# Kernel tuning notes

Hardware: AMD Instinct MI355X
Metric: run time of the kernel (lower is better)

Reference implementation:

```python
import jax, jax.numpy as jnp
import numpy as np

B, T, C = 2, 2048, 1024
H = 16
HD = C // H  # head_size = 64
FF = 4 * C
EPS = 1e-5


def layernorm(x, g, b):
    mu = jnp.mean(x, axis=-1, keepdims=True)
    var = jnp.mean(jnp.square(x - mu), axis=-1, keepdims=True)
    return (x - mu) * jax.lax.rsqrt(var + EPS) * g + b


def setup_inputs() -> dict:
    key = jax.random.key(0)
    ks = jax.random.split(key, 12)
    s_c = 1.0 / np.sqrt(C)
    s_hc = 1.0 / np.sqrt(C)
    s_ff = 1.0 / np.sqrt(FF)
    return {
        "x": jax.random.normal(ks[0], (B, T, C), jnp.float32),
        "Wq": jax.random.normal(ks[1], (H, C, HD), jnp.float32) * s_hc,
        "Wk": jax.random.normal(ks[2], (H, C, HD), jnp.float32) * s_hc,
        "Wv": jax.random.normal(ks[3], (H, C, HD), jnp.float32) * s_hc,
        "Wo": jax.random.normal(ks[4], (C, C), jnp.float32) * s_c,
        "bo": jax.random.normal(ks[5], (C,), jnp.float32) * 0.01,
        "W1": jax.random.normal(ks[6], (C, FF), jnp.float32) * s_c,
        "b1": jax.random.normal(ks[7], (FF,), jnp.float32) * 0.01,
        "W2": jax.random.normal(ks[8], (FF, C), jnp.float32) * s_ff,
        "b2": jax.random.normal(ks[9], (C,), jnp.float32) * 0.01,
        "g1": jnp.ones((C,), jnp.float32),
        "be1": jnp.zeros((C,), jnp.float32),
        "g2": jnp.ones((C,), jnp.float32),
        "be2": jnp.zeros((C,), jnp.float32),
    }


def reference(x, Wq, Wk, Wv, Wo, bo, W1, b1, W2, b2, g1, be1, g2, be2):
    # --- self-attention sublayer (pre-LN, residual) ---
    h = layernorm(x, g1, be1)                               # [B,T,C]
    q = jnp.einsum("btc,hcd->bhtd", h, Wq)                   # [B,H,T,HD]
    k = jnp.einsum("btc,hcd->bhtd", h, Wk)
    v = jnp.einsum("btc,hcd->bhtd", h, Wv)
    scores = jnp.einsum("bhtd,bhsd->bhts", q, k) * (HD ** -0.5)
    causal = jnp.tril(jnp.ones((T, T), bool))
    scores = jnp.where(causal, scores, -jnp.inf)
    wei = jax.nn.softmax(scores, axis=-1)                    # [B,H,T,T]
    attn = jnp.einsum("bhts,bhsd->bhtd", wei, v)             # [B,H,T,HD]
    attn = attn.transpose(0, 2, 1, 3).reshape(B, T, H * HD)  # concat heads
    x = x + attn @ Wo + bo
    # --- feedforward sublayer (pre-LN, residual) ---
    h2 = layernorm(x, g2, be2)
    x = x + jax.nn.relu(h2 @ W1 + b1) @ W2 + b2
    return x
```

## Files before the change

kernel.cpp:

```cpp
#include <hip/hip_runtime.h>
#include <hip/hip_bf16.h>
#include <cstdint>
#include <cstddef>
#include <cstring>

#define B_ 2
#define T_ 2048
#define C_ 1024
#define H_ 16
#define HD_ 64
#define FF_ 4096
#define BT_ (B_*T_)

typedef __attribute__((ext_vector_type(8))) short short8;
typedef __attribute__((ext_vector_type(4))) float f32x4;

__device__ __forceinline__ float bf2f(ushort u) {
    return __uint_as_float(((uint)u) << 16);
}
__device__ __forceinline__ ushort f2bf(float f) {
    uint x = __float_as_uint(f);
    return (ushort)((x + 0x7fffu + ((x >> 16) & 1u)) >> 16);
}
__device__ __forceinline__ ushort f2bf_hw(float f) {
    __hip_bfloat16 h = __float2bfloat16(f);
    ushort u;
    __builtin_memcpy(&u, &h, 2);
    return u;
}

#define GLDS16(g, l)                                                        \
    __builtin_amdgcn_global_load_lds(                                       \
        (const __attribute__((address_space(1))) void*)(g),                 \
        (__attribute__((address_space(3))) void*)(l), 16, 0, 0)

__global__ __launch_bounds__(256) void ln_kernel(const float* __restrict__ x,
                                                 const float* __restrict__ g,
                                                 const float* __restrict__ b,
                                                 ushort* __restrict__ out) {
    int row = blockIdx.x;
    int tid = threadIdx.x;
    const float* xr = x + (size_t)row * C_;
    float4 v = *(const float4*)(xr + tid * 4);
    float s = v.x + v.y + v.z + v.w;
    float q = v.x*v.x + v.y*v.y + v.z*v.z + v.w*v.w;
    #pragma unroll
    for (int off = 32; off > 0; off >>= 1) {
        s += __shfl_down(s, off);
        q += __shfl_down(q, off);
    }
    __shared__ float ss[4], qs[4];
    if ((tid & 63) == 0) { ss[tid >> 6] = s; qs[tid >> 6] = q; }
    __syncthreads();
    s = ss[0] + ss[1] + ss[2] + ss[3];
    q = qs[0] + qs[1] + qs[2] + qs[3];
    float mu  = s * (1.0f / C_);
    float var = q * (1.0f / C_) - mu * mu;
    float r = rsqrtf(var + 1e-5f);
    float4 gv = *(const float4*)(g + tid * 4);
    float4 bv = *(const float4*)(b + tid * 4);
    ushort4 o;
    o.x = f2bf((v.x - mu) * r * gv.x + bv.x);
    o.y = f2bf((v.y - mu) * r * gv.y + bv.y);
    o.z = f2bf((v.z - mu) * r * gv.z + bv.z);
    o.w = f2bf((v.w - mu) * r * gv.w + bv.w);
    *(ushort4*)(out + (size_t)row * C_ + tid * 4) = o;
}

__global__ __launch_bounds__(256) void tcvt_w(const float* __restrict__ Wo,
                                              const float* __restrict__ W1,
                                              const float* __restrict__ W2,
                                              ushort* __restrict__ Wo_t,
                                              ushort* __restrict__ W1_t,
                                              ushort* __restrict__ W2_t) {
    __shared__ float tile[32][33];
    int fb = blockIdx.x;
    const float* in;
    ushort* out;
    int Cc, ldo, bx, by;
    if (fb < 1024) {
        in = Wo; out = Wo_t; Cc = 1024; ldo = 1024;
        bx = fb & 31; by = fb >> 5;
    } else if (fb < 5120) {
        int t = fb - 1024;
        in = W1; out = W1_t; Cc = 4096; ldo = 1024;
        bx = t & 127; by = t >> 7;
    } else {
        int t = fb - 5120;
        in = W2; out = W2_t; Cc = 1024; ldo = 4096;
        bx = t & 31; by = t >> 5;
    }
    int c0 = bx * 32, r0 = by * 32;
    int tx = threadIdx.x & 31, ty = threadIdx.x >> 5;
    #pragma unroll
    for (int i = 0; i < 4; i++) {
        int r = ty + i * 8;
        tile[r][tx] = in[(size_t)(r0 + r) * Cc + c0 + tx];
    }
    __syncthreads();
    #pragma unroll
    for (int i = 0; i < 4; i++) {
        int c = ty + i * 8;
        out[(size_t)(c0 + c) * ldo + r0 + tx] = f2bf(tile[tx][c]);
    }
}

__global__ __launch_bounds__(256) void tcvt_qkv(const float* __restrict__ Wq,
                                                const float* __restrict__ Wk,
                                                const float* __restrict__ Wv,
                                                ushort* __restrict__ qkvw) {
    __shared__ float tile[32][33];
    int z = blockIdx.z;
    const float* in = (z < 16 ? Wq : (z < 32 ? Wk : Wv)) + (size_t)(z & 15) * 65536;
    ushort* out = qkvw + (size_t)z * 65536;
    int c0 = blockIdx.x * 32, r0 = blockIdx.y * 32;
    #pragma unroll
    for (int i = 0; i < 4; i++) {
        int r = threadIdx.y + i * 8;
        tile[r][threadIdx.x] = in[(size_t)(r0 + r) * 64 + c0 + threadIdx.x];
    }
    __syncthreads();
    #pragma unroll
    for (int i = 0; i < 4; i++) {
        int c = threadIdx.y + i * 8;
        out[(size_t)(c0 + c) * 1024 + r0 + threadIdx.x] = f2bf(tile[threadIdx.x][c]);
    }
}

template<int EPI, bool OUT_BF16>
__global__ __launch_bounds__(512, 4) void gemm2(
    const ushort* __restrict__ A,
    const ushort* __restrict__ Bt,
    void* __restrict__ Cout,
    const float* __restrict__ bias,
    const float* __restrict__ resid,
    int M, int N, int K, int KS)
{
    __shared__ ushort As[3][128 * 32];
    __shared__ ushort Bs[3][256 * 32];

    int gx = gridDim.x;
    int nwg = gx * gridDim.y;
    int bid = blockIdx.y * gx + blockIdx.x;
    int cpx = nwg >> 3;
    int swz = (bid & 7) * cpx + (bid >> 3);
    int bx = swz % gx, by = swz / gx;

    int tid  = threadIdx.x;
    int lane = tid & 63;
    int lr = lane & 15, lq = lane >> 4;
    int wave = tid >> 6;
    int wr = wave >> 2, wc = wave & 3;
    int m0 = by * 128, n0 = bx * 256;
    int Koff = blockIdx.z * KS;
    size_t zoff = (size_t)blockIdx.z * ((size_t)M * N);

    f32x4 acc[4][4];
    #pragma unroll
    for (int i = 0; i < 4; i++)
        #pragma unroll
        for (int j = 0; j < 4; j++)
            acc[i][j] = {0.f, 0.f, 0.f, 0.f};

    int srow = tid >> 2;
    int scol = ((tid & 3) ^ ((srow >> 1) & 3)) * 8;
    const ushort* gA  = A  + (size_t)(m0 + srow) * K + Koff + scol;
    const ushort* gB0 = Bt + (size_t)(n0 + srow) * K + Koff + scol;
    const ushort* gB1 = Bt + (size_t)(n0 + 128 + srow) * K + Koff + scol;
    int NT = KS / 32;

    auto stage = [&](int kt, int buf) {
        int off = kt * 32;
        GLDS16(gA + off,  (char*)As[buf] + wave * 1024);
        GLDS16(gB0 + off, (char*)Bs[buf] + wave * 1024);
        GLDS16(gB1 + off, (char*)Bs[buf] + 8192 + wave * 1024);
    };

    stage(0, 0);
    stage(1, 1);
    asm volatile("s_waitcnt vmcnt(3)" ::: "memory");
    __builtin_amdgcn_s_barrier();

    int so = (lq ^ ((lr >> 1) & 3)) << 4;

    int cur = 0;
    for (int t = 0; t < NT; ++t) {
        const char* Ab = (const char*)As[cur] + (wr * 64 + lr) * 64 + so;
        const char* Bb = (const char*)Bs[cur] + (wc * 64 + lr) * 64 + so;

        short8 a[4], b[4];
        #pragma unroll
        for (int fr = 0; fr < 4; fr++)
            a[fr] = *(const short8*)(Ab + fr * 1024);
        #pragma unroll
        for (int fc = 0; fc < 4; fc++)
            b[fc] = *(const short8*)(Bb + fc * 1024);

        if (t + 2 < NT) {
            int nb = cur + 2;
            if (nb >= 3) nb -= 3;
            stage(t + 2, nb);
        }

        #pragma unroll
        for (int fr = 0; fr < 4; fr++)
            #pragma unroll
            for (int fc = 0; fc < 4; fc++)
                acc[fr][fc] = __builtin_amdgcn_mfma_f32_16x16x32_bf16(
                    a[fr], b[fc], acc[fr][fc], 0, 0, 0);

        if (t + 1 == NT) break;
        if (t + 2 < NT)
            asm volatile("s_waitcnt vmcnt(3)" ::: "memory");
        else
            asm volatile("s_waitcnt vmcnt(0)" ::: "memory");
        __builtin_amdgcn_s_barrier();
        cur = (cur == 2) ? 0 : cur + 1;
    }

    #pragma unroll
    for (int fr = 0; fr < 4; fr++) {
        #pragma unroll
        for (int fc = 0; fc < 4; fc++) {
            int col = n0 + wc * 64 + fc * 16 + lr;
            #pragma unroll
            for (int j = 0; j < 4; j++) {
                int row = m0 + wr * 64 + fr * 16 + lq * 4 + j;
                float v = acc[fr][fc][j];
                if (EPI & 1) v += bias[col];
                if (EPI & 2) v = fmaxf(v, 0.f);
                if (EPI & 4) v += resid[(size_t)row * N + col];
                if (OUT_BF16)
                    ((ushort*)Cout)[zoff + (size_t)row * N + col] = f2bf(v);
                else
                    ((float*)Cout)[zoff + (size_t)row * N + col] = v;
            }
        }
    }
}

__global__ __launch_bounds__(512, 4) void gemm_qkvt(
    const ushort* __restrict__ h_bf,
    const ushort* __restrict__ qkvw,
    ushort* __restrict__ qk_act,
    ushort* __restrict__ p_vt)
{
    __shared__ ushort As[3][128 * 32];
    __shared__ ushort Bs[3][256 * 32];

    const ushort* A; const ushort* Bt; ushort* Cb;
    int N, K, KS, gx, nwg, bid, Koff;
    size_t zoff;
    int fb = blockIdx.x;
    if (fb < 256) {
        A = h_bf; Bt = qkvw; Cb = qk_act;
        N = 2048; K = C_; KS = C_;
        gx = 8; nwg = 256; bid = fb; Koff = 0; zoff = 0;
    } else {
        int local = fb - 256;
        int z = local >> 7;
        A = qkvw + (size_t)2 * 1024 * 1024; Bt = h_bf; Cb = p_vt;
        N = BT_; K = C_; KS = 512;
        gx = 16; nwg = 128; bid = local & 127;
        Koff = z * 512; zoff = (size_t)z * ((size_t)1024 * BT_);
    }
    int cpx = nwg >> 3;
    int swz = (bid & 7) * cpx + (bid >> 3);
    int bx = swz % gx, by = swz / gx;

    int tid  = threadIdx.x;
    int lane = tid & 63;
    int lr = lane & 15, lq = lane >> 4;
    int wave = tid >> 6;
    int wr = wave >> 2, wc = wave & 3;
    int m0 = by * 128, n0 = bx * 256;

    f32x4 acc[4][4];
    #pragma unroll
    for (int i = 0; i < 4; i++)
        #pragma unroll
        for (int j = 0; j < 4; j++)
            acc[i][j] = {0.f, 0.f, 0.f, 0.f};

    int srow = tid >> 2;
    int scol = ((tid & 3) ^ ((srow >> 1) & 3)) * 8;
    const ushort* gA  = A  + (size_t)(m0 + srow) * K + Koff + scol;
    const ushort* gB0 = Bt + (size_t)(n0 + srow) * K + Koff + scol;
    const ushort* gB1 = Bt + (size_t)(n0 + 128 + srow) * K + Koff + scol;
    int NT = KS / 32;

    auto stage = [&](int kt, int buf) {
        int off = kt * 32;
        GLDS16(gA + off,  (char*)As[buf] + wave * 1024);
        GLDS16(gB0 + off, (char*)Bs[buf] + wave * 1024);
        GLDS16(gB1 + off, (char*)Bs[buf] + 8192 + wave * 1024);
    };

    stage(0, 0);
    stage(1, 1);
    asm volatile("s_waitcnt vmcnt(3)" ::: "memory");
    __builtin_amdgcn_s_barrier();

    int so = (lq ^ ((lr >> 1) & 3)) << 4;

    int cur = 0;
    for (int t = 0; t < NT; ++t) {
        const char* Ab = (const char*)As[cur] + (wr * 64 + lr) * 64 + so;
        const char* Bb = (const char*)Bs[cur] + (wc * 64 + lr) * 64 + so;

        short8 a[4], b[4];
        #pragma unroll
        for (int fr = 0; fr < 4; fr++)
            a[fr] = *(const short8*)(Ab + fr * 1024);
        #pragma unroll
        for (int fc = 0; fc < 4; fc++)
            b[fc] = *(const short8*)(Bb + fc * 1024);

        if (t + 2 < NT) {
            int nb = cur + 2;
            if (nb >= 3) nb -= 3;
            stage(t + 2, nb);
        }

        #pragma unroll
        for (int fr = 0; fr < 4; fr++)
            #pragma unroll
            for (int fc = 0; fc < 4; fc++)
                acc[fr][fc] = __builtin_amdgcn_mfma_f32_16x16x32_bf16(
                    a[fr], b[fc], acc[fr][fc], 0, 0, 0);

        if (t + 1 == NT) break;
        if (t + 2 < NT)
            asm volatile("s_waitcnt vmcnt(3)" ::: "memory");
        else
            asm volatile("s_waitcnt vmcnt(0)" ::: "memory");
        __builtin_amdgcn_s_barrier();
        cur = (cur == 2) ? 0 : cur + 1;
    }

    #pragma unroll
    for (int fr = 0; fr < 4; fr++) {
        #pragma unroll
        for (int fc = 0; fc < 4; fc++) {
            int col = n0 + wc * 64 + fc * 16 + lr;
            #pragma unroll
            for (int j = 0; j < 4; j++) {
                int row = m0 + wr * 64 + fr * 16 + lq * 4 + j;
                Cb[zoff + (size_t)row * N + col] = f2bf(acc[fr][fc][j]);
            }
        }
    }
}

__global__ __launch_bounds__(256) void vt_red(ushort* __restrict__ vt,
                                              const ushort* __restrict__ p) {
    size_t i = (size_t)blockIdx.x * 256 + threadIdx.x;
    ushort4 a = ((const ushort4*)p)[i];
    ushort4 b = ((const ushort4*)(p + (size_t)1024 * BT_))[i];
    ushort4 o;
    o.x = f2bf(bf2f(a.x) + bf2f(b.x));
    o.y = f2bf(bf2f(a.y) + bf2f(b.y));
    o.z = f2bf(bf2f(a.z) + bf2f(b.z));
    o.w = f2bf(bf2f(a.w) + bf2f(b.w));
    ((ushort4*)vt)[i] = o;
}

__global__ __launch_bounds__(256) void wo_ln(float* __restrict__ out,
                                             ushort* __restrict__ h,
                                             const ushort* __restrict__ p,
                                             const float* __restrict__ bo,
                                             const float* __restrict__ x,
                                             const float* __restrict__ g,
                                             const float* __restrict__ be) {
    int row = blockIdx.x;
    int tid = threadIdx.x;
    size_t base = (size_t)row * C_ + tid * 4;
    float4 v = *(const float4*)(x + base);
    float4 c = *(const float4*)(bo + tid * 4);
    #pragma unroll
    for (int z = 0; z < 4; z++) {
        ushort4 a = *(const ushort4*)(p + (size_t)z * BT_ * C_ + base);
        v.x += bf2f(a.x); v.y += bf2f(a.y);
        v.z += bf2f(a.z); v.w += bf2f(a.w);
    }
    v.x += c.x; v.y += c.y; v.z += c.z; v.w += c.w;
    *(float4*)(out + base) = v;

    float s = v.x + v.y + v.z + v.w;
    float q = v.x*v.x + v.y*v.y + v.z*v.z + v.w*v.w;
    #pragma unroll
    for (int off = 32; off > 0; off >>= 1) {
        s += __shfl_down(s, off);
        q += __shfl_down(q, off);
    }
    __shared__ float ss[4], qs[4];
    if ((tid & 63) == 0) { ss[tid >> 6] = s; qs[tid >> 6] = q; }
    __syncthreads();
    s = ss[0] + ss[1] + ss[2] + ss[3];
    q = qs[0] + qs[1] + qs[2] + qs[3];
    float mu  = s * (1.0f / C_);
    float var = q * (1.0f / C_) - mu * mu;
    float r = rsqrtf(var + 1e-5f);
    float4 gv = *(const float4*)(g + tid * 4);
    float4 bv = *(const float4*)(be + tid * 4);
    ushort4 o;
    o.x = f2bf((v.x - mu) * r * gv.x + bv.x);
    o.y = f2bf((v.y - mu) * r * gv.y + bv.y);
    o.z = f2bf((v.z - mu) * r * gv.z + bv.z);
    o.w = f2bf((v.w - mu) * r * gv.w + bv.w);
    *(ushort4*)(h + base) = o;
}

__global__ __launch_bounds__(256) void ff2_red4(float* __restrict__ out,
                                                const ushort* __restrict__ p,
                                                const float* __restrict__ b2) {
    size_t i = (size_t)blockIdx.x * 256 + threadIdx.x;
    float4 o = ((float4*)out)[i];
    float4 c = ((const float4*)b2)[i & 255];
    #pragma unroll
    for (int z = 0; z < 4; z++) {
        ushort4 a = ((const ushort4*)(p + (size_t)z * BT_ * C_))[i];
        o.x += bf2f(a.x); o.y += bf2f(a.y);
        o.z += bf2f(a.z); o.w += bf2f(a.w);
    }
    o.x += c.x; o.y += c.y; o.z += c.z; o.w += c.w;
    ((float4*)out)[i] = o;
}

__global__ __launch_bounds__(256, 3) void attn_mfma(const ushort* __restrict__ qk,
                                                    const ushort* __restrict__ vt,
                                                    ushort* __restrict__ Opart,
                                                    float* __restrict__ ml) {
    const float C2 = 0.18033688011f;
    const float THR2 = 12.0f;

    int flat = blockIdx.x;
    int xcd = flat & 7;
    int idx = flat >> 3;
    int bh  = xcd * 4 + (idx & 3);
    int qz  = idx >> 2;
    int qa  = 15 - (qz >> 1);
    int z   = qz & 1;

    int bb = bh >> 4;
    int head = bh & 15;
    int q0 = qa * 128;

    int tid  = threadIdx.x;
    int lane = tid & 63;
    int lr = lane & 15, lq = lane >> 4;
    int wave = tid >> 6;
    int qw = q0 + wave * 32;

    __shared__ ushort Ks[2][64 * 64];
    __shared__ ushort Vs[2][64 * 64];
    __shared__ ushort Ps[4][32 * 64];
    char* pw = (char*)Ps[wave];

    short8 qf[2][2];
    {
        const ushort* qb = qk + ((size_t)(bb * T_ + qw)) * 2048 + head * 64;
        #pragma unroll
        for (int mt = 0; mt < 2; mt++)
            #pragma unroll
            for (int kk = 0; kk < 2; kk++)
                qf[mt][kk] = *(const short8*)(qb + (size_t)(mt*16 + lr) * 2048 + kk*32 + lq*8);
    }

    f32x4 acc[2][4];
    f32x4 lsum[2];
    float m2[2][4];
    #pragma unroll
    for (int mt = 0; mt < 2; mt++) {
        #pragma unroll
        for (int dt = 0; dt < 4; dt++) acc[mt][dt] = {0.f, 0.f, 0.f, 0.f};
        lsum[mt] = {0.f, 0.f, 0.f, 0.f};
        #pragma unroll
        for (int j = 0; j < 4; j++) m2[mt][j] = -INFINITY;
    }

    const short8 onesf = {(short)0x3F80, (short)0x3F80, (short)0x3F80, (short)0x3F80,
                          (short)0x3F80, (short)0x3F80, (short)0x3F80, (short)0x3F80};

    int srow = tid >> 3;
    int ssc = ((tid & 7) ^ (srow & 7)) * 8;
    const ushort* kg0 = qk + ((size_t)(bb * T_ + srow)) * 2048 + 1024 + head * 64 + ssc;
    const ushort* vg0 = vt + ((size_t)(head * 64 + srow)) * 4096 + (size_t)bb * 2048 + ssc;

    auto stage = [&](int it, int buf) {
        int s0 = it * 64;
        char* Kb = (char*)Ks[buf] + wave * 1024;
        char* Vb = (char*)Vs[buf] + wave * 1024;
        GLDS16(kg0 + (size_t)s0 * 2048,        Kb);
        GLDS16(kg0 + (size_t)(s0 + 32) * 2048, Kb + 4096);
        GLDS16(vg0 + s0,                        Vb);
        GLDS16(vg0 + (size_t)32 * 4096 + s0,    Vb + 4096);
    };

    int nt = 2 * (qa + 1);
    stage(z, 0);
    __syncthreads();
    int cur = 0;

    for (int it = z; it < nt; it += 2) {
        if (it + 2 < nt) stage(it + 2, cur ^ 1);

        int s0h = it * 64;
        if (s0h <= qw + 31) {
            const ushort* Kc = Ks[cur];
            const ushort* Vc = Vs[cur];

            f32x4 sa[2][4];
            __builtin_amdgcn_s_setprio(1);
            #pragma unroll
            for (int n = 0; n < 4; n++) {
                int row = n*16 + lr;
                const char* kbase = (const char*)Kc + row*128;
                short8 kf0 = *(const short8*)(kbase + ((lq       ^ (row & 7)) << 4));
                short8 kf1 = *(const short8*)(kbase + (((4 + lq) ^ (row & 7)) << 4));
                #pragma unroll
                for (int mt = 0; mt < 2; mt++) {
                    f32x4 tq = {0.f, 0.f, 0.f, 0.f};
                    tq = __builtin_amdgcn_mfma_f32_16x16x32_bf16(qf[mt][0], kf0, tq, 0, 0, 0);
                    tq = __builtin_amdgcn_mfma_f32_16x16x32_bf16(qf[mt][1], kf1, tq, 0, 0, 0);
                    sa[mt][n] = tq;
                }
            }
            __builtin_amdgcn_s_setprio(0);

            if (s0h + 63 > qw) {
                #pragma unroll
                for (int mt = 0; mt < 2; mt++)
                    #pragma unroll
                    for (int n = 0; n < 4; n++)
                        #pragma unroll
                        for (int j = 0; j < 4; j++) {
                            int scolm = s0h + n*16 + lr;
                            int qrow = qw + mt*16 + lq*4 + j;
                            if (scolm > qrow) sa[mt][n][j] = -INFINITY;
                        }
            }

            float vmax2[2][4];
            bool growf = false;
            #pragma unroll
            for (int mt = 0; mt < 2; mt++) {
                #pragma unroll
                for (int j = 0; j < 4; j++) {
                    float v = fmaxf(fmaxf(sa[mt][0][j], sa[mt][1][j]),
                                    fmaxf(sa[mt][2][j], sa[mt][3][j]));
                    #pragma unroll
                    for (int off = 1; off < 16; off <<= 1)
                        v = fmaxf(v, __shfl_xor(v, off));
                    float v2 = v * C2;
                    vmax2[mt][j] = v2;
                    growf |= (v2 > m2[mt][j] + THR2);
                }
            }
            if (__any(growf)) {
                #pragma unroll
                for (int mt = 0; mt < 2; mt++)
                    #pragma unroll
                    for (int j = 0; j < 4; j++) {
                        float m2n = fmaxf(m2[mt][j], vmax2[mt][j]);
                        float corr = __builtin_amdgcn_exp2f(m2[mt][j] - m2n);
                        m2[mt][j] = m2n;
                        lsum[mt][j] *= corr;
                        #pragma unroll
                        for (int dt = 0; dt < 4; dt++)
                            acc[mt][dt][j] *= corr;
                    }
            }

            #pragma unroll
            for (int mt = 0; mt < 2; mt++)
                #pragma unroll
                for (int n = 0; n < 4; n++)
                    #pragma unroll
                    for (int j = 0; j < 4; j++) {
                        float p = __builtin_amdgcn_exp2f(
                            fmaf(sa[mt][n][j], C2, -m2[mt][j]));
                        int row = mt*16 + lq*4 + j;
                        int col = n*16 + lr;
                        int byte = row*128 + ((((col >> 3) ^ (row & 7))) << 4) + (col & 7)*2;
                        *(ushort*)(pw + byte) = f2bf_hw(p);
                    }

            short8 pf[2][2];
            #pragma unroll
            for (int mt = 0; mt < 2; mt++) {
                int row = mt*16 + lr;
                #pragma unroll
                for (int kk = 0; kk < 2; kk++)
                    pf[mt][kk] = *(const short8*)(pw + row*128
                                   + (((kk*4 + lq) ^ (row & 7)) << 4));
            }
            __builtin_amdgcn_s_setprio(1);
            #pragma unroll
            for (int kk = 0; kk < 2; kk++)
                #pragma unroll
                for (int mt = 0; mt < 2; mt++)
                    lsum[mt] = __builtin_amdgcn_mfma_f32_16x16x32_bf16(
                        pf[mt][kk], onesf, lsum[mt], 0, 0, 0);
            #pragma unroll
            for (int dt = 0; dt < 4; dt++) {
                int row = dt*16 + lr;
                const char* vbase = (const char*)Vc + row*128;
                #pragma unroll
                for (int kk = 0; kk < 2; kk++) {
                    short8 vf = *(const short8*)(vbase
                                  + (((kk*4 + lq) ^ (row & 7)) << 4));
                    #pragma unroll
                    for (int mt = 0; mt < 2; mt++)
                        acc[mt][dt] = __builtin_amdgcn_mfma_f32_16x16x32_bf16(
                            pf[mt][kk], vf, acc[mt][dt], 0, 0, 0);
                }
            }
            __builtin_amdgcn_s_setprio(0);
        }

        __syncthreads();
        cur ^= 1;
    }

    ushort* ob = Opart + (size_t)z * ((size_t)BT_ * C_)
               + ((size_t)(bb * T_ + qw)) * 1024 + head * 64;
    #pragma unroll
    for (int mt = 0; mt < 2; mt++)
        #pragma unroll
        for (int j = 0; j < 4; j++) {
            float l = lsum[mt][j];
            float inv = l > 0.f ? 1.0f / l : 0.f;
            #pragma unroll
            for (int dt = 0; dt < 4; dt++)
                ob[(size_t)(mt*16 + lq*4 + j) * 1024 + dt*16 + lr] =
                    f2bf(acc[mt][dt][j] * inv);
        }
    if (lr == 0) {
        float* mlz = ml + ((size_t)(z * 16 + head)) * (BT_ * 2);
        #pragma unroll
        for (int mt = 0; mt < 2; mt++)
            #pragma unroll
            for (int j = 0; j < 4; j++) {
                size_t row = (size_t)(bb * T_ + qw + mt*16 + lq*4 + j);
                *(float2*)(mlz + row * 2) = make_float2(m2[mt][j], lsum[mt][j]);
            }
    }
}

__global__ __launch_bounds__(256) void attn_comb(const ushort* __restrict__ Opart,
                                                 const float* __restrict__ ml,
                                                 ushort* __restrict__ outb) {
    int row = blockIdx.x;
    int tid = threadIdx.x;
    int col = tid * 4;
    int head = col >> 6;
    float2 ml0 = *(const float2*)(ml + ((size_t)head * BT_ + row) * 2);
    float2 ml1 = *(const float2*)(ml + ((size_t)(16 + head) * BT_ + row) * 2);
    float m = fmaxf(ml0.x, ml1.x);
    float w0 = ml0.y * __builtin_amdgcn_exp2f(ml0.x - m);
    float w1 = ml1.y * __builtin_amdgcn_exp2f(ml1.x - m);
    float inv = 1.0f / (w0 + w1);
    w0 *= inv; w1 *= inv;
    size_t idx = (size_t)row * C_ + col;
    ushort4 a = *(const ushort4*)(Opart + idx);
    ushort4 b = *(const ushort4*)(Opart + (size_t)BT_ * C_ + idx);
    ushort4 o;
    o.x = f2bf(bf2f(a.x) * w0 + bf2f(b.x) * w1);
    o.y = f2bf(bf2f(a.y) * w0 + bf2f(b.y) * w1);
    o.z = f2bf(bf2f(a.z) * w0 + bf2f(b.z) * w1);
    o.w = f2bf(bf2f(a.w) * w0 + bf2f(b.w) * w1);
    *(ushort4*)(outb + idx) = o;
}

extern "C" void kernel_launch(void* const* d_in, const int* in_sizes, int n_in,
                              void* d_out, int out_size, void* d_ws, size_t ws_size,
                              hipStream_t stream) {
    const float* x   = (const float*)d_in[0];
    const float* Wq  = (const float*)d_in[1];
    const float* Wk  = (const float*)d_in[2];
    const float* Wv  = (const float*)d_in[3];
    const float* Wo  = (const float*)d_in[4];
    const float* bo  = (const float*)d_in[5];
    const float* W1  = (const float*)d_in[6];
    const float* b1  = (const float*)d_in[7];
    const float* W2  = (const float*)d_in[8];
    const float* b2  = (const float*)d_in[9];
    const float* g1  = (const float*)d_in[10];
    const float* be1 = (const float*)d_in[11];
    const float* g2  = (const float*)d_in[12];
    const float* be2 = (const float*)d_in[13];
    float* out = (float*)d_out;

    char* ws = (char*)d_ws;
    const size_t MB = 1 << 20;
    ushort* h_bf    = (ushort*)(ws);
    ushort* qk_act  = (ushort*)(ws + 8*MB);
    ushort* vt      = (ushort*)(ws + 24*MB);
    ushort* attn_bf = (ushort*)(ws);
    ushort* W2_t    = (ushort*)(ws + 40*MB);
    ushort* qkvw    = (ushort*)(ws + 48*MB);
    ushort* Wo_t    = (ushort*)(ws + 54*MB);
    ushort* W1_t    = (ushort*)(ws + 56*MB);
    ushort* p_vt    = (ushort*)(ws + 64*MB);
    ushort* Opart   = (ushort*)(ws + 64*MB);
    float*  mlbuf   = (float*)(ws + 80*MB);
    ushort* p_wo    = (ushort*)(ws + 8*MB);
    ushort* ff1     = (ushort*)(ws + 8*MB);
    ushort* p_ff2   = (ushort*)(ws + 48*MB);

    tcvt_qkv<<<dim3(2, 32, 48), dim3(32, 8), 0, stream>>>(Wq, Wk, Wv, qkvw);
    tcvt_w<<<dim3(9216), dim3(256), 0, stream>>>(Wo, W1, W2, Wo_t, W1_t, W2_t);

    ln_kernel<<<dim3(BT_), dim3(256), 0, stream>>>(x, g1, be1, h_bf);

    gemm_qkvt<<<dim3(512), dim3(512), 0, stream>>>(h_bf, qkvw, qk_act, p_vt);
    vt_red<<<dim3(1024*BT_/4/256), dim3(256), 0, stream>>>(vt, p_vt);

    attn_mfma<<<dim3(1024), dim3(256), 0, stream>>>(qk_act, vt, Opart, mlbuf);
    attn_comb<<<dim3(BT_), dim3(256), 0, stream>>>(Opart, mlbuf, attn_bf);

    gemm2<0, true><<<dim3(1024/256, BT_/128, 4), dim3(512), 0, stream>>>(
        attn_bf, Wo_t, p_wo, nullptr, nullptr, BT_, C_, C_, 256);
    wo_ln<<<dim3(BT_), dim3(256), 0, stream>>>(out, h_bf, p_wo, bo, x, g2, be2);

    gemm2<1|2, true><<<dim3(FF_/256, BT_/128, 1), dim3(512), 0, stream>>>(
        h_bf, W1_t, ff1, b1, nullptr, BT_, FF_, C_, C_);

    gemm2<0, true><<<dim3(1024/256, BT_/128, 4), dim3(512), 0, stream>>>(
        ff1, W2_t, p_ff2, nullptr, nullptr, BT_, C_, FF_, 1024);
    ff2_red4<<<dim3(BT_*C_/4/256), dim3(256), 0, stream>>>(out, p_ff2, b2);
}
```

Before: 235.5 us.

## Merge weight conversion and LN1 into one prep kernel; drop V split-K

Folds the QKV weight transpose, the Wo/W1/W2 transpose-convert and the first layernorm into a single prep kernel, cutting two launches. The V-transpose part of the QKV GEMM no longer uses 2-way split-K with a separate bf16 reduction kernel. Instead 128 blocks run the full K=1024 and write vt directly. This removes the partial-buffer traffic, the vt_red launch and a double bf16 rounding, but leaves fewer blocks (384 vs 512) with longer K loops for the V part.

Result: faster. 226.1 us (median of 2 runs) (-4.0%).

```diff
diff --git a/kernel.cpp b/kernel.cpp
--- a/kernel.cpp
+++ b/kernel.cpp
@@ -34,64 +34,75 @@
         (const __attribute__((address_space(1))) void*)(g),                 \
         (__attribute__((address_space(3))) void*)(l), 16, 0, 0)
 
-__global__ __launch_bounds__(256) void ln_kernel(const float* __restrict__ x,
-                                                 const float* __restrict__ g,
-                                                 const float* __restrict__ b,
-                                                 ushort* __restrict__ out) {
-    int row = blockIdx.x;
+__global__ __launch_bounds__(256) void prep(
+    const float* __restrict__ Wq, const float* __restrict__ Wk,
+    const float* __restrict__ Wv, const float* __restrict__ Wo,
+    const float* __restrict__ W1, const float* __restrict__ W2,
+    const float* __restrict__ x,  const float* __restrict__ g1,
+    const float* __restrict__ be1,
+    ushort* __restrict__ qkvw, ushort* __restrict__ Wo_t,
+    ushort* __restrict__ W1_t, ushort* __restrict__ W2_t,
+    ushort* __restrict__ h_bf)
+{
+    int fb = blockIdx.x;
     int tid = threadIdx.x;
-    const float* xr = x + (size_t)row * C_;
-    float4 v = *(const float4*)(xr + tid * 4);
-    float s = v.x + v.y + v.z + v.w;
-    float q = v.x*v.x + v.y*v.y + v.z*v.z + v.w*v.w;
-    #pragma unroll
-    for (int off = 32; off > 0; off >>= 1) {
-        s += __shfl_down(s, off);
-        q += __shfl_down(q, off);
-    }
+    __shared__ float tile[32][33];
     __shared__ float ss[4], qs[4];
-    if ((tid & 63) == 0) { ss[tid >> 6] = s; qs[tid >> 6] = q; }
-    __syncthreads();
-    s = ss[0] + ss[1] + ss[2] + ss[3];
-    q = qs[0] + qs[1] + qs[2] + qs[3];
-    float mu  = s * (1.0f / C_);
-    float var = q * (1.0f / C_) - mu * mu;
-    float r = rsqrtf(var + 1e-5f);
-    float4 gv = *(const float4*)(g + tid * 4);
-    float4 bv = *(const float4*)(b + tid * 4);
-    ushort4 o;
-    o.x = f2bf((v.x - mu) * r * gv.x + bv.x);
-    o.y = f2bf((v.y - mu) * r * gv.y + bv.y);
-    o.z = f2bf((v.z - mu) * r * gv.z + bv.z);
-    o.w = f2bf((v.w - mu) * r * gv.w + bv.w);
-    *(ushort4*)(out + (size_t)row * C_ + tid * 4) = o;
-}
-
-__global__ __launch_bounds__(256) void tcvt_w(const float* __restrict__ Wo,
-                                              const float* __restrict__ W1,
-                                              const float* __restrict__ W2,
-                                              ushort* __restrict__ Wo_t,
-                                              ushort* __restrict__ W1_t,
-                                              ushort* __restrict__ W2_t) {
-    __shared__ float tile[32][33];
-    int fb = blockIdx.x;
+
+    if (fb >= 12288) {
+        int row = fb - 12288;
+        const float* xr = x + (size_t)row * C_;
+        float4 v = *(const float4*)(xr + tid * 4);
+        float s = v.x + v.y + v.z + v.w;
+        float q = v.x*v.x + v.y*v.y + v.z*v.z + v.w*v.w;
+        #pragma unroll
+        for (int off = 32; off > 0; off >>= 1) {
+            s += __shfl_down(s, off);
+            q += __shfl_down(q, off);
+        }
+        if ((tid & 63) == 0) { ss[tid >> 6] = s; qs[tid >> 6] = q; }
+        __syncthreads();
+        s = ss[0] + ss[1] + ss[2] + ss[3];
+        q = qs[0] + qs[1] + qs[2] + qs[3];
+        float mu  = s * (1.0f / C_);
+        float var = q * (1.0f / C_) - mu * mu;
+        float r = rsqrtf(var + 1e-5f);
+        float4 gv = *(const float4*)(g1 + tid * 4);
+        float4 bv = *(const float4*)(be1 + tid * 4);
+        ushort4 o;
+        o.x = f2bf((v.x - mu) * r * gv.x + bv.x);
+        o.y = f2bf((v.y - mu) * r * gv.y + bv.y);
+        o.z = f2bf((v.z - mu) * r * gv.z + bv.z);
+        o.w = f2bf((v.w - mu) * r * gv.w + bv.w);
+        *(ushort4*)(h_bf + (size_t)row * C_ + tid * 4) = o;
+        return;
+    }
+
     const float* in;
     ushort* out;
     int Cc, ldo, bx, by;
-    if (fb < 1024) {
+    if (fb < 3072) {
+        int z = fb >> 6;
+        int rem = fb & 63;
+        in = (z < 16 ? Wq : (z < 32 ? Wk : Wv)) + (size_t)(z & 15) * 65536;
+        out = qkvw + (size_t)z * 65536;
+        Cc = 64; ldo = 1024;
+        bx = rem & 1; by = rem >> 1;
+    } else if (fb < 4096) {
+        int t = fb - 3072;
         in = Wo; out = Wo_t; Cc = 1024; ldo = 1024;
-        bx = fb & 31; by = fb >> 5;
-    } else if (fb < 5120) {
-        int t = fb - 1024;
+        bx = t & 31; by = t >> 5;
+    } else if (fb < 8192) {
+        int t = fb - 4096;
         in = W1; out = W1_t; Cc = 4096; ldo = 1024;
         bx = t & 127; by = t >> 7;
     } else {
-        int t = fb - 5120;
+        int t = fb - 8192;
         in = W2; out = W2_t; Cc = 1024; ldo = 4096;
         bx = t & 31; by = t >> 5;
     }
     int c0 = bx * 32, r0 = by * 32;
-    int tx = threadIdx.x & 31, ty = threadIdx.x >> 5;
+    int tx = tid & 31, ty = tid >> 5;
     #pragma unroll
     for (int i = 0; i < 4; i++) {
         int r = ty + i * 8;
@@ -102,28 +113,6 @@
     for (int i = 0; i < 4; i++) {
         int c = ty + i * 8;
         out[(size_t)(c0 + c) * ldo + r0 + tx] = f2bf(tile[tx][c]);
-    }
-}
-
-__global__ __launch_bounds__(256) void tcvt_qkv(const float* __restrict__ Wq,
-                                                const float* __restrict__ Wk,
-                                                const float* __restrict__ Wv,
-                                                ushort* __restrict__ qkvw) {
-    __shared__ float tile[32][33];
-    int z = blockIdx.z;
-    const float* in = (z < 16 ? Wq : (z < 32 ? Wk : Wv)) + (size_t)(z & 15) * 65536;
-    ushort* out = qkvw + (size_t)z * 65536;
-    int c0 = blockIdx.x * 32, r0 = blockIdx.y * 32;
-    #pragma unroll
-    for (int i = 0; i < 4; i++) {
-        int r = threadIdx.y + i * 8;
-        tile[r][threadIdx.x] = in[(size_t)(r0 + r) * 64 + c0 + threadIdx.x];
-    }
-    __syncthreads();
-    #pragma unroll
-    for (int i = 0; i < 4; i++) {
-        int c = threadIdx.y + i * 8;
-        out[(size_t)(c0 + c) * 1024 + r0 + threadIdx.x] = f2bf(tile[threadIdx.x][c]);
     }
 }
 
@@ -243,27 +232,22 @@
     const ushort* __restrict__ h_bf,
     const ushort* __restrict__ qkvw,
     ushort* __restrict__ qk_act,
-    ushort* __restrict__ p_vt)
+    ushort* __restrict__ vt)
 {
     __shared__ ushort As[3][128 * 32];
     __shared__ ushort Bs[3][256 * 32];
 
     const ushort* A; const ushort* Bt; ushort* Cb;
-    int N, K, KS, gx, nwg, bid, Koff;
-    size_t zoff;
+    int N, gx, nwg, bid;
     int fb = blockIdx.x;
     if (fb < 256) {
         A = h_bf; Bt = qkvw; Cb = qk_act;
-        N = 2048; K = C_; KS = C_;
-        gx = 8; nwg = 256; bid = fb; Koff = 0; zoff = 0;
+        N = 2048; gx = 8; nwg = 256; bid = fb;
     } else {
-        int local = fb - 256;
-        int z = local >> 7;
-        A = qkvw + (size_t)2 * 1024 * 1024; Bt = h_bf; Cb = p_vt;
-        N = BT_; K = C_; KS = 512;
-        gx = 16; nwg = 128; bid = local & 127;
-        Koff = z * 512; zoff = (size_t)z * ((size_t)1024 * BT_);
-    }
+        A = qkvw + (size_t)2 * 1024 * 1024; Bt = h_bf; Cb = vt;
+        N = BT_; gx = 16; nwg = 128; bid = fb - 256;
+    }
+    const int K = C_;
     int cpx = nwg >> 3;
     int swz = (bid & 7) * cpx + (bid >> 3);
     int bx = swz % gx, by = swz / gx;
@@ -284,10 +268,10 @@
 
     int srow = tid >> 2;
     int scol = ((tid & 3) ^ ((srow >> 1) & 3)) * 8;
-    const ushort* gA  = A  + (size_t)(m0 + srow) * K + Koff + scol;
-    const ushort* gB0 = Bt + (size_t)(n0 + srow) * K + Koff + scol;
-    const ushort* gB1 = Bt + (size_t)(n0 + 128 + srow) * K + Koff + scol;
-    int NT = KS / 32;
+    const ushort* gA  = A  + (size_t)(m0 + srow) * K + scol;
+    const ushort* gB0 = Bt + (size_t)(n0 + srow) * K + scol;
+    const ushort* gB1 = Bt + (size_t)(n0 + 128 + srow) * K + scol;
+    const int NT = 32;
 
     auto stage = [&](int kt, int buf) {
         int off = kt * 32;
@@ -346,23 +330,10 @@
             #pragma unroll
             for (int j = 0; j < 4; j++) {
                 int row = m0 + wr * 64 + fr * 16 + lq * 4 + j;
-                Cb[zoff + (size_t)row * N + col] = f2bf(acc[fr][fc][j]);
+                Cb[(size_t)row * N + col] = f2bf(acc[fr][fc][j]);
             }
         }
     }
-}
-
-__global__ __launch_bounds__(256) void vt_red(ushort* __restrict__ vt,
-                                              const ushort* __restrict__ p) {
-    size_t i = (size_t)blockIdx.x * 256 + threadIdx.x;
-    ushort4 a = ((const ushort4*)p)[i];
-    ushort4 b = ((const ushort4*)(p + (size_t)1024 * BT_))[i];
-    ushort4 o;
-    o.x = f2bf(bf2f(a.x) + bf2f(b.x));
-    o.y = f2bf(bf2f(a.y) + bf2f(b.y));
-    o.z = f2bf(bf2f(a.z) + bf2f(b.z));
-    o.w = f2bf(bf2f(a.w) + bf2f(b.w));
-    ((ushort4*)vt)[i] = o;
 }
 
 __global__ __launch_bounds__(256) void wo_ln(float* __restrict__ out,
@@ -702,20 +673,17 @@
     ushort* qkvw    = (ushort*)(ws + 48*MB);
     ushort* Wo_t    = (ushort*)(ws + 54*MB);
     ushort* W1_t    = (ushort*)(ws + 56*MB);
-    ushort* p_vt    = (ushort*)(ws + 64*MB);
     ushort* Opart   = (ushort*)(ws + 64*MB);
     float*  mlbuf   = (float*)(ws + 80*MB);
     ushort* p_wo    = (ushort*)(ws + 8*MB);
     ushort* ff1     = (ushort*)(ws + 8*MB);
     ushort* p_ff2   = (ushort*)(ws + 48*MB);
 
-    tcvt_qkv<<<dim3(2, 32, 48), dim3(32, 8), 0, stream>>>(Wq, Wk, Wv, qkvw);
-    tcvt_w<<<dim3(9216), dim3(256), 0, stream>>>(Wo, W1, W2, Wo_t, W1_t, W2_t);
-
-    ln_kernel<<<dim3(BT_), dim3(256), 0, stream>>>(x, g1, be1, h_bf);
-
-    gemm_qkvt<<<dim3(512), dim3(512), 0, stream>>>(h_bf, qkvw, qk_act, p_vt);
-    vt_red<<<dim3(1024*BT_/4/256), dim3(256), 0, stream>>>(vt, p_vt);
+    prep<<<dim3(16384), dim3(256), 0, stream>>>(
+        Wq, Wk, Wv, Wo, W1, W2, x, g1, be1,
+        qkvw, Wo_t, W1_t, W2_t, h_bf);
+
+    gemm_qkvt<<<dim3(384), dim3(512), 0, stream>>>(h_bf, qkvw, qk_act, vt);
 
     attn_mfma<<<dim3(1024), dim3(256), 0, stream>>>(qk_act, vt, Opart, mlbuf);
     attn_comb<<<dim3(BT_), dim3(256), 0, stream>>>(Opart, mlbuf, attn_bf);
```
